# Optimization experiments

Hardware: AMD Instinct MI355X
Metric: run time of the kernel (lower is better)

## Reference

```python
import jax, jax.numpy as jnp
import numpy as np

H = 768
NH = 12
HD = 64
FF = 3072
EPS = 1e-12


def layer_norm(x, g, b):
    mu = jnp.mean(x, axis=-1, keepdims=True)
    var = jnp.mean((x - mu) ** 2, axis=-1, keepdims=True)
    return (x - mu) * jax.lax.rsqrt(var + EPS) * g + b


def setup_inputs() -> dict:
    key = jax.random.key(0)
    ks = jax.random.split(key, 16)
    B, S, L = 16, 512, 50
    s = 0.02
    return {
        "hidden_states": jax.random.normal(ks[0], (B, S, H), jnp.float32),
        "attention_mask": jnp.zeros((B, 1, 1, S), jnp.float32),
        "past_key": jax.random.normal(ks[1], (B, NH, L, HD), jnp.float32),
        "past_value": jax.random.normal(ks[2], (B, NH, L, HD), jnp.float32),
        "Wq": jax.random.normal(ks[3], (H, H), jnp.float32) * s,
        "bq": jnp.zeros((H,), jnp.float32),
        "Wk": jax.random.normal(ks[4], (H, H), jnp.float32) * s,
        "bk": jnp.zeros((H,), jnp.float32),
        "Wv": jax.random.normal(ks[5], (H, H), jnp.float32) * s,
        "bv": jnp.zeros((H,), jnp.float32),
        "Wo": jax.random.normal(ks[6], (H, H), jnp.float32) * s,
        "bo": jnp.zeros((H,), jnp.float32),
        "ln1_g": jnp.ones((H,), jnp.float32),
        "ln1_b": jnp.zeros((H,), jnp.float32),
        "Wi": jax.random.normal(ks[7], (H, FF), jnp.float32) * s,
        "bi": jnp.zeros((FF,), jnp.float32),
        "Wf": jax.random.normal(ks[8], (FF, H), jnp.float32) * s,
        "bf": jnp.zeros((H,), jnp.float32),
        "ln2_g": jnp.ones((H,), jnp.float32),
        "ln2_b": jnp.zeros((H,), jnp.float32),
    }


def reference(hidden_states, attention_mask, past_key, past_value,
              Wq, bq, Wk, bk, Wv, bv, Wo, bo, ln1_g, ln1_b,
              Wi, bi, Wf, bf, ln2_g, ln2_b):
    B, S, _ = hidden_states.shape
    L = past_key.shape[2]

    def heads(x):  # [B,S,H] -> [B,NH,S,HD]
        return x.reshape(B, S, NH, HD).transpose(0, 2, 1, 3)

    q = heads(hidden_states @ Wq + bq)
    k = heads(hidden_states @ Wk + bk)
    v = heads(hidden_states @ Wv + bv)

    # faithful to source bug: past_key_values[0] concatenated into BOTH k and v
    k = jnp.concatenate([past_key, k], axis=2)  # [B,NH,L+S,HD]
    v = jnp.concatenate([past_key, v], axis=2)

    scores = jnp.einsum('bhqd,bhkd->bhqk', q, k) / jnp.sqrt(jnp.float32(HD))
    # visual mask positions get +1.0 (torch.ones), faithful to source
    vis_mask = jnp.ones((B, 1, 1, L), scores.dtype)
    full_mask = jnp.concatenate([vis_mask, attention_mask], axis=-1)
    scores = scores + full_mask

    probs = jax.nn.softmax(scores, axis=-1)
    ctx = jnp.einsum('bhqk,bhkd->bhqd', probs, v)  # [B,NH,S,HD]
    ctx = ctx.transpose(0, 2, 1, 3).reshape(B, S, H)

    attn_out = layer_norm(ctx @ Wo + bo + hidden_states, ln1_g, ln1_b)

    inter = jax.nn.gelu(attn_out @ Wi + bi, approximate=False)
    layer_out = layer_norm(inter @ Wf + bf + attn_out, ln2_g, ln2_b)
    return layer_out
```

## Files before the change

### kernel.cpp

```cpp
#include <hip/hip_runtime.h>
#include <math.h>

#define HDIM 64
#define NHEAD 12
#define HDN 768
#define QKVN 2304
#define FFDIM 3072
#define LPAST 50
#define SEQ 512
#define NBATCH 16
#define TKV (LPAST + SEQ)
#define TKVP 576
#define MTOK (NBATCH * SEQ)
#define NBH (NBATCH * NHEAD)

typedef __attribute__((ext_vector_type(8))) short short8;
typedef __attribute__((ext_vector_type(4))) float f32x4;

__device__ __forceinline__ ushort f2bf(float x) {
    union { float f; unsigned u; } c; c.f = x;
    unsigned r = (c.u + 0x7fffu + ((c.u >> 16) & 1u)) >> 16;
    return (ushort)r;
}
__device__ __forceinline__ float bf2f(ushort u) { return __uint_as_float((unsigned)u << 16); }
__device__ __forceinline__ float geluf(float v) {
    return 0.5f * v * (1.0f + erff(v * 0.70710678118654752f));
}

#define GLOAD_LDS16(gsrc, ldst)                                                    \
    __builtin_amdgcn_global_load_lds(                                              \
        (const __attribute__((address_space(1))) void*)(gsrc),                     \
        (__attribute__((address_space(3))) void*)(ldst), 16, 0, 0)

__global__ __launch_bounds__(256) void cast_bf(const float* __restrict__ x,
                                               ushort* __restrict__ y, int n4) {
    int i = blockIdx.x * 256 + threadIdx.x;
    if (i >= n4) return;
    float4 v = ((const float4*)x)[i];
    ushort4 o; o.x = f2bf(v.x); o.y = f2bf(v.y); o.z = f2bf(v.z); o.w = f2bf(v.w);
    ((ushort4*)y)[i] = o;
}

__global__ __launch_bounds__(256) void pack_bias(const float* __restrict__ bq,
                                                 const float* __restrict__ bk,
                                                 const float* __restrict__ bv,
                                                 float* __restrict__ o) {
    int i = blockIdx.x * 256 + threadIdx.x;
    if (i >= QKVN) return;
    o[i] = i < HDN ? bq[i] : (i < 2 * HDN ? bk[i - HDN] : bv[i - 2 * HDN]);
}

__global__ __launch_bounds__(256) void transpose_cast(const float* __restrict__ W,
                                                      ushort* __restrict__ WT,
                                                      int K, int N) {
    __shared__ float t[32][33];
    const int n0 = blockIdx.x * 32, k0 = blockIdx.y * 32;
    const int tx = threadIdx.x & 31, ty = threadIdx.x >> 5;
    #pragma unroll
    for (int i = 0; i < 4; ++i)
        t[ty + i * 8][tx] = W[(size_t)(k0 + ty + i * 8) * N + n0 + tx];
    __syncthreads();
    #pragma unroll
    for (int i = 0; i < 4; ++i)
        WT[(size_t)(n0 + ty + i * 8) * K + k0 + tx] = f2bf(t[tx][ty + i * 8]);
}

__global__ __launch_bounds__(256) void transpose_cast4(
    const float* __restrict__ W0, const float* __restrict__ W1,
    const float* __restrict__ W2, const float* __restrict__ W3,
    ushort* __restrict__ T0, ushort* __restrict__ T1,
    ushort* __restrict__ T2, ushort* __restrict__ T3) {
    __shared__ float t[32][33];
    const int z = blockIdx.z;
    const float* W = z == 0 ? W0 : z == 1 ? W1 : z == 2 ? W2 : W3;
    ushort* WT = z == 0 ? T0 : z == 1 ? T1 : z == 2 ? T2 : T3;
    const int n0 = blockIdx.x * 32, k0 = blockIdx.y * 32;
    const int tx = threadIdx.x & 31, ty = threadIdx.x >> 5;
    #pragma unroll
    for (int i = 0; i < 4; ++i)
        t[ty + i * 8][tx] = W[(size_t)(k0 + ty + i * 8) * HDN + n0 + tx];
    __syncthreads();
    #pragma unroll
    for (int i = 0; i < 4; ++i)
        WT[(size_t)(n0 + ty + i * 8) * HDN + k0 + tx] = f2bf(t[tx][ty + i * 8]);
}

template<int EPI>
__global__ __launch_bounds__(256) void gemm_mfma3(
    const ushort* __restrict__ A, const ushort* __restrict__ B,
    int lda, int ldb,
    const float* __restrict__ bias, const float* __restrict__ resid,
    const ushort* __restrict__ resid_bf,
    void* __restrict__ Cout, int M, int N, int K)
{
    __shared__ ushort sm[3 * 8192];

    const int tid = threadIdx.x;
    const int lane = tid & 63;
    const int wv = tid >> 6;
    const int wr = wv >> 1, wc = wv & 1;
    const int bm = blockIdx.x * 128, bn = blockIdx.y * 128;
    const int lr = lane & 15, lg = lane >> 4;
    const int swzu = ((lr * 64 + lg * 16) ^ ((lr & 8) << 2)) >> 1;

    int srow[2], skk[2];
    #pragma unroll
    for (int r = 0; r < 2; ++r) {
        int o = (tid + 256 * r) * 16;
        int st = o >> 10;
        int q = o & 1023;
        q ^= ((q >> 9) & 1) << 5;
        srow[r] = st * 16 + (q >> 6);
        skk[r] = (q & 63) >> 1;
    }
    const ushort* Abase = A + (size_t)bm * lda;
    const ushort* Bbase = B + (size_t)bn * ldb;
    const int nt = K >> 5;

    f32x4 acc[4][4] = {};

#define STAGE(T, BUF)                                                            \
    do {                                                                         \
        const int k0_ = (T) << 5;                                                \
        ushort* base_ = sm + (BUF) * 8192;                                       \
        _Pragma("unroll")                                                        \
        for (int r_ = 0; r_ < 2; ++r_) {                                         \
            int sl_ = tid + 256 * r_;                                            \
            GLOAD_LDS16(Abase + (size_t)srow[r_] * lda + k0_ + skk[r_],          \
                        (char*)base_ + sl_ * 16);                                \
        }                                                                        \
        _Pragma("unroll")                                                        \
        for (int r_ = 0; r_ < 2; ++r_) {                                         \
            int sl_ = tid + 256 * r_;                                            \
            GLOAD_LDS16(Bbase + (size_t)srow[r_] * ldb + k0_ + skk[r_],          \
                        (char*)(base_ + 4096) + sl_ * 16);                       \
        }                                                                        \
    } while (0)

    STAGE(0, 0);
    STAGE(1, 1);
    asm volatile("s_waitcnt vmcnt(4)" ::: "memory");
    __builtin_amdgcn_sched_barrier(0);
    __builtin_amdgcn_s_barrier();
    __builtin_amdgcn_sched_barrier(0);

    int buf = 0;
    for (int t = 0; t < nt; ++t) {
        if (t + 2 < nt) {
            int nbuf = buf + 2; if (nbuf >= 3) nbuf -= 3;
            STAGE(t + 2, nbuf);
        }
        const ushort* ab = sm + buf * 8192;
        short8 af[4], bfv[4];
        #pragma unroll
        for (int i = 0; i < 4; ++i) {
            af[i]  = *(const short8*)(ab + (wr * 4 + i) * 512 + swzu);
            bfv[i] = *(const short8*)(ab + 4096 + (wc * 4 + i) * 512 + swzu);
        }
        __builtin_amdgcn_s_setprio(1);
        #pragma unroll
        for (int i = 0; i < 4; ++i)
            #pragma unroll
            for (int j = 0; j < 4; ++j)
                acc[i][j] = __builtin_amdgcn_mfma_f32_16x16x32_bf16(
                    af[i], bfv[j], acc[i][j], 0, 0, 0);
        __builtin_amdgcn_s_setprio(0);
        if (t + 2 < nt)
            asm volatile("s_waitcnt vmcnt(4)" ::: "memory");
        else
            asm volatile("s_waitcnt vmcnt(0)" ::: "memory");
        __builtin_amdgcn_sched_barrier(0);
        __builtin_amdgcn_s_barrier();
        __builtin_amdgcn_sched_barrier(0);
        buf = buf + 1 == 3 ? 0 : buf + 1;
    }
#undef STAGE

    #pragma unroll
    for (int i = 0; i < 4; ++i) {
        #pragma unroll
        for (int j = 0; j < 4; ++j) {
            const int col = bn + wc * 64 + j * 16 + lr;
            const float bv = bias[col];
            #pragma unroll
            for (int rr = 0; rr < 4; ++rr) {
                const int row = bm + wr * 64 + i * 16 + (lane >> 4) * 4 + rr;
                const size_t idx = (size_t)row * N + col;
                float v = acc[i][j][rr] + bv;
                if (EPI == 0) {
                    ((ushort*)Cout)[idx] = f2bf(v);
                } else if (EPI == 1) {
                    ((float*)Cout)[idx] = v + resid[idx];
                } else if (EPI == 2) {
                    ((ushort*)Cout)[idx] = f2bf(geluf(v));
                } else {
                    ((float*)Cout)[idx] = v + bf2f(resid_bf[idx]);
                }
            }
        }
    }
}

__global__ __launch_bounds__(256) void kvK(
    const ushort* __restrict__ qkv, const float* __restrict__ past_key,
    ushort* __restrict__ kf)
{
    const size_t total = (size_t)NBH * TKV * HDIM;
    size_t idx = (size_t)blockIdx.x * 256 + threadIdx.x;
    if (idx >= total) return;
    int d = idx & 63;
    size_t r = idx >> 6;
    int t = (int)(r % TKV);
    int bh = (int)(r / TKV);
    ushort kv_;
    if (t < LPAST) {
        kv_ = f2bf(past_key[((size_t)bh * LPAST + t) * HDIM + d]);
    } else {
        int b = bh / NHEAD, h = bh % NHEAD;
        kv_ = qkv[((size_t)(b * SEQ + (t - LPAST))) * QKVN + HDN + h * HDIM + d];
    }
    kf[idx] = kv_;
}

__global__ __launch_bounds__(256) void kvVT(
    const ushort* __restrict__ qkv, const float* __restrict__ past_key,
    ushort* __restrict__ vt)
{
    __shared__ ushort td[64][72];
    const int bh = blockIdx.x / 9;
    const int t0 = (blockIdx.x % 9) * 64;
    const int b = bh / NHEAD, h = bh % NHEAD;
    const int trow = threadIdx.x >> 2, seg = threadIdx.x & 3;
    const int t = t0 + trow;

    ushort vals[16];
    if (t < LPAST) {
        const float* pk = past_key + ((size_t)bh * LPAST + t) * HDIM + seg * 16;
        #pragma unroll
        for (int i = 0; i < 4; ++i) {
            float4 f = ((const float4*)pk)[i];
            vals[i * 4 + 0] = f2bf(f.x); vals[i * 4 + 1] = f2bf(f.y);
            vals[i * 4 + 2] = f2bf(f.z); vals[i * 4 + 3] = f2bf(f.w);
        }
    } else if (t < TKV) {
        const ushort* vp = qkv + ((size_t)(b * SEQ + (t - LPAST))) * QKVN
                               + 2 * HDN + h * HDIM + seg * 16;
        uint4 u0 = ((const uint4*)vp)[0], u1 = ((const uint4*)vp)[1];
        *(uint4*)&vals[0] = u0; *(uint4*)&vals[8] = u1;
    } else {
        #pragma unroll
        for (int i = 0; i < 16; ++i) vals[i] = 0;
    }
    #pragma unroll
    for (int i = 0; i < 16; ++i) td[trow][seg * 16 + i] = vals[i];
    __syncthreads();

    const int d = threadIdx.x >> 2;
    ushort o[16];
    #pragma unroll
    for (int i = 0; i < 16; ++i) o[i] = td[seg * 16 + i][d];
    ushort* dst = vt + ((size_t)bh * HDIM + d) * TKVP + t0 + seg * 16;
    *(uint4*)dst = *(uint4*)&o[0];
    *(uint4*)(dst + 8) = *(uint4*)&o[8];
}

__global__ __launch_bounds__(256) void attn3(
    const ushort* __restrict__ qkv, const ushort* __restrict__ kf,
    const ushort* __restrict__ vt, const float* __restrict__ mask,
    ushort* __restrict__ ctx)
{
    __shared__ ushort Ks[64 * 64];
    __shared__ ushort Vs[64 * 64];
    __shared__ ushort Ps[4][16 * 64];

    const int wv = threadIdx.x >> 6, lane = threadIdx.x & 63;
    const int lr = lane & 15, lg = lane >> 4;
    const int bid = blockIdx.x;
    const int xcd = bid & 7, gi = bid >> 3;
    const int bh = xcd * (NBH / 8) + (gi >> 3);
    const int s0 = (gi & 7) * 64;
    const int b = bh / NHEAD, h = bh % NHEAD;

    short8 af[2];
    {
        const ushort* qp = qkv + ((size_t)(b * SEQ + s0 + wv * 16 + lr)) * QKVN
                               + h * HDIM + lg * 8;
        af[0] = *(const short8*)qp;
        af[1] = *(const short8*)(qp + 32);
    }

    const ushort* kbase = kf + (size_t)bh * TKV * HDIM;
    const ushort* vbase = vt + (size_t)bh * HDIM * TKVP;

    float m[4] = {-1e30f, -1e30f, -1e30f, -1e30f};
    float l[4] = {};
    f32x4 ctxa[4] = {};

    for (int kt = 0; kt < 9; ++kt) {
        const int t0 = kt * 64;
        #pragma unroll
        for (int r = 0; r < 2; ++r) {
            int sl = (int)threadIdx.x + 256 * r;
            int row = sl >> 3, p = sl & 7;
            int j = p ^ (row & 7);
            int trow = t0 + row; if (trow > TKV - 1) trow = TKV - 1;
            GLOAD_LDS16(kbase + ((size_t)trow << 6) + j * 8, (char*)Ks + sl * 16);
        }
        #pragma unroll
        for (int r = 0; r < 2; ++r) {
            int sl = (int)threadIdx.x + 256 * r;
            int row = sl >> 3, p = sl & 7;
            int j = p ^ (row & 7);
            GLOAD_LDS16(vbase + (size_t)row * TKVP + t0 + j * 8, (char*)Vs + sl * 16);
        }
        __syncthreads();

        f32x4 sa[4] = {};
        #pragma unroll
        for (int kb = 0; kb < 4; ++kb) {
            const int key = kb * 16 + lr;
            #pragma unroll
            for (int c = 0; c < 2; ++c) {
                const int phys = (c * 4 + lg) ^ (key & 7);
                short8 kfrag = *(const short8*)&Ks[key * 64 + phys * 8];
                sa[kb] = __builtin_amdgcn_mfma_f32_16x16x32_bf16(
                    af[c], kfrag, sa[kb], 0, 0, 0);
            }
        }

        float scv[4][4];
        #pragma unroll
        for (int kb = 0; kb < 4; ++kb) {
            const int t = t0 + kb * 16 + lr;
            float add = 0.0f;
            bool dead = (t >= TKV);
            if (!dead) add = (t < LPAST) ? 1.0f : mask[(size_t)b * SEQ + (t - LPAST)];
            #pragma unroll
            for (int r = 0; r < 4; ++r)
                scv[kb][r] = dead ? -1e30f : fmaf(sa[kb][r], 0.125f, add);
        }

        #pragma unroll
        for (int r = 0; r < 4; ++r) {
            float mx = fmaxf(fmaxf(scv[0][r], scv[1][r]), fmaxf(scv[2][r], scv[3][r]));
            mx = fmaxf(mx, __shfl_xor(mx, 1));
            mx = fmaxf(mx, __shfl_xor(mx, 2));
            mx = fmaxf(mx, __shfl_xor(mx, 4));
            mx = fmaxf(mx, __shfl_xor(mx, 8));
            const float mn = fmaxf(m[r], mx);
            const float f = __expf(m[r] - mn);
            m[r] = mn;
            l[r] *= f;
            #pragma unroll
            for (int dg = 0; dg < 4; ++dg) ctxa[dg][r] *= f;
            const int q_ = lg * 4 + r;
            #pragma unroll
            for (int kb = 0; kb < 4; ++kb) {
                float p = __expf(scv[kb][r] - mn);
                l[r] += p;
                const int key = kb * 16 + lr;
                const int phys = (key >> 3) ^ (q_ & 7);
                Ps[wv][q_ * 64 + phys * 8 + (key & 7)] = f2bf(p);
            }
        }

        short8 pa[2];
        #pragma unroll
        for (int c = 0; c < 2; ++c) {
            const int phys = (c * 4 + lg) ^ (lr & 7);
            pa[c] = *(const short8*)&Ps[wv][lr * 64 + phys * 8];
        }
        #pragma unroll
        for (int dg = 0; dg < 4; ++dg) {
            const int d = dg * 16 + lr;
            #pragma unroll
            for (int c = 0; c < 2; ++c) {
                const int phys = (c * 4 + lg) ^ (d & 7);
                short8 vfrag = *(const short8*)&Vs[d * 64 + phys * 8];
                ctxa[dg] = __builtin_amdgcn_mfma_f32_16x16x32_bf16(
                    pa[c], vfrag, ctxa[dg], 0, 0, 0);
            }
        }
        __syncthreads();
    }

    #pragma unroll
    for (int r = 0; r < 4; ++r) {
        float s = l[r];
        s += __shfl_xor(s, 1); s += __shfl_xor(s, 2);
        s += __shfl_xor(s, 4); s += __shfl_xor(s, 8);
        l[r] = 1.0f / s;
    }
    #pragma unroll
    for (int r = 0; r < 4; ++r) {
        const int q_ = s0 + wv * 16 + lg * 4 + r;
        const size_t base = ((size_t)(b * SEQ + q_)) * HDN + h * HDIM;
        #pragma unroll
        for (int dg = 0; dg < 4; ++dg)
            ctx[base + dg * 16 + lr] = f2bf(ctxa[dg][r] * l[r]);
    }
}

__global__ __launch_bounds__(256) void layernorm2(
    const float* __restrict__ x, const float* __restrict__ g,
    const float* __restrict__ b, float* __restrict__ out,
    ushort* __restrict__ out_bf)
{
    const size_t row = blockIdx.x;
    const float* xr = &x[row * HDN];
    const int t = threadIdx.x;

    float v0 = xr[t], v1 = xr[t + 256], v2 = xr[t + 512];

    __shared__ float red[4];
    float s = v0 + v1 + v2;
    #pragma unroll
    for (int off = 32; off > 0; off >>= 1) s += __shfl_xor(s, off);
    if ((t & 63) == 0) red[t >> 6] = s;
    __syncthreads();
    float mean = (red[0] + red[1] + red[2] + red[3]) * (1.0f / 768.0f);

    float d0 = v0 - mean, d1 = v1 - mean, d2 = v2 - mean;
    float vs = d0 * d0 + d1 * d1 + d2 * d2;
    #pragma unroll
    for (int off = 32; off > 0; off >>= 1) vs += __shfl_xor(vs, off);
    __syncthreads();
    if ((t & 63) == 0) red[t >> 6] = vs;
    __syncthreads();
    float var = (red[0] + red[1] + red[2] + red[3]) * (1.0f / 768.0f);
    float rstd = rsqrtf(var + 1e-12f);

    float o0 = d0 * rstd * g[t] + b[t];
    float o1 = d1 * rstd * g[t + 256] + b[t + 256];
    float o2 = d2 * rstd * g[t + 512] + b[t + 512];
    if (out) {
        out[row * HDN + t] = o0;
        out[row * HDN + t + 256] = o1;
        out[row * HDN + t + 512] = o2;
    }
    if (out_bf) {
        out_bf[row * HDN + t] = f2bf(o0);
        out_bf[row * HDN + t + 256] = f2bf(o1);
        out_bf[row * HDN + t + 512] = f2bf(o2);
    }
}

extern "C" void kernel_launch(void* const* d_in, const int* in_sizes, int n_in,
                              void* d_out, int out_size, void* d_ws, size_t ws_size,
                              hipStream_t stream) {
    const float* hs       = (const float*)d_in[0];
    const float* mask     = (const float*)d_in[1];
    const float* past_key = (const float*)d_in[2];
    const float* Wq = (const float*)d_in[4];
    const float* bq = (const float*)d_in[5];
    const float* Wk = (const float*)d_in[6];
    const float* bk = (const float*)d_in[7];
    const float* Wv = (const float*)d_in[8];
    const float* bv = (const float*)d_in[9];
    const float* Wo = (const float*)d_in[10];
    const float* bo = (const float*)d_in[11];
    const float* ln1_g = (const float*)d_in[12];
    const float* ln1_b = (const float*)d_in[13];
    const float* Wi = (const float*)d_in[14];
    const float* bi = (const float*)d_in[15];
    const float* Wf = (const float*)d_in[16];
    const float* bf_ = (const float*)d_in[17];
    const float* ln2_g = (const float*)d_in[18];
    const float* ln2_b = (const float*)d_in[19];
    float* out = (float*)d_out;

    char* w = (char*)d_ws;
    ushort* WqT   = (ushort*)(w + 0);
    ushort* WoT   = (ushort*)(w + 3538944);
    ushort* WiT   = (ushort*)(w + 4718592);
    ushort* WfT   = (ushort*)(w + 9437184);
    float*  bqkv  = (float*)(w + 14155776);
    ushort* hs_bf = (ushort*)(w + 14172160);
    ushort* qkv   = (ushort*)(w + 26755072);
    ushort* kf    = (ushort*)(w + 64503808);
    ushort* vt    = (ushort*)(w + 78315520);
    ushort* ctx_bf = hs_bf;
    float*  tmp   = (float*)(w + 64503808);
    ushort* inter = (ushort*)(w + 14172160);
    ushort* aln_bf = (ushort*)(w + 89669632);
    ushort* WkT = WqT + (size_t)HDN * HDN;
    ushort* WvT = WqT + (size_t)2 * HDN * HDN;

    dim3 b256(256);

    cast_bf<<<dim3((MTOK * HDN / 4 + 255) / 256), b256, 0, stream>>>(hs, hs_bf, MTOK * HDN / 4);
    pack_bias<<<dim3(9), b256, 0, stream>>>(bq, bk, bv, bqkv);
    transpose_cast4<<<dim3(24, 24, 4), b256, 0, stream>>>(Wq, Wk, Wv, Wo, WqT, WkT, WvT, WoT);
    transpose_cast<<<dim3(96, 24), b256, 0, stream>>>(Wi, WiT, HDN, FFDIM);
    transpose_cast<<<dim3(24, 96), b256, 0, stream>>>(Wf, WfT, FFDIM, HDN);

    gemm_mfma3<0><<<dim3(MTOK / 128, QKVN / 128), b256, 0, stream>>>(
        hs_bf, WqT, HDN, HDN, bqkv, nullptr, nullptr, qkv, MTOK, QKVN, HDN);

    {
        size_t ktot = (size_t)NBH * TKV * HDIM;
        kvK<<<dim3((unsigned)((ktot + 255) / 256)), b256, 0, stream>>>(qkv, past_key, kf);
    }
    kvVT<<<dim3(NBH * 9), b256, 0, stream>>>(qkv, past_key, vt);

    attn3<<<dim3(NBH * 8), b256, 0, stream>>>(qkv, kf, vt, mask, ctx_bf);

    gemm_mfma3<1><<<dim3(MTOK / 128, HDN / 128), b256, 0, stream>>>(
        ctx_bf, WoT, HDN, HDN, bo, hs, nullptr, tmp, MTOK, HDN, HDN);
    layernorm2<<<dim3(MTOK), b256, 0, stream>>>(tmp, ln1_g, ln1_b, nullptr, aln_bf);

    gemm_mfma3<2><<<dim3(MTOK / 128, FFDIM / 128), b256, 0, stream>>>(
        aln_bf, WiT, HDN, HDN, bi, nullptr, nullptr, inter, MTOK, FFDIM, HDN);
    gemm_mfma3<4><<<dim3(MTOK / 128, HDN / 128), b256, 0, stream>>>(
        inter, WfT, FFDIM, FFDIM, bf_, nullptr, aln_bf, tmp, MTOK, HDN, FFDIM);

    layernorm2<<<dim3(MTOK), b256, 0, stream>>>(tmp, ln2_g, ln2_b, out, nullptr);
}
```

Measured before the change: 275.1 us.

## Widen GEMM tiles to 128x256, merge prep and KV kernels, bf16 residual temporaries

Five preprocessing launches become one prep kernel, and the K-copy and V-transpose kernels merge into kvAll. The GEMM now uses a 128x256 tile, with each wave covering all 128 rows and 64 columns, held in 72KB of dynamic LDS at two blocks per CU. Residual-sum temporaries for both layernorms move from fp32 to bf16, which halves their memory traffic. The changes aim to cut launch overhead and memory traffic and to raise operand reuse per LDS load, at the cost of more registers, fewer blocks for the N=768 GEMMs, and bf16 rounding before layernorm.

```diff
diff --git a/kernel.cpp b/kernel.cpp
--- a/kernel.cpp
+++ b/kernel.cpp
@@ -32,114 +32,115 @@
         (const __attribute__((address_space(1))) void*)(gsrc),                     \
         (__attribute__((address_space(3))) void*)(ldst), 16, 0, 0)
 
-__global__ __launch_bounds__(256) void cast_bf(const float* __restrict__ x,
-                                               ushort* __restrict__ y, int n4) {
-    int i = blockIdx.x * 256 + threadIdx.x;
-    if (i >= n4) return;
-    float4 v = ((const float4*)x)[i];
-    ushort4 o; o.x = f2bf(v.x); o.y = f2bf(v.y); o.z = f2bf(v.z); o.w = f2bf(v.w);
-    ((ushort4*)y)[i] = o;
-}
-
-__global__ __launch_bounds__(256) void pack_bias(const float* __restrict__ bq,
-                                                 const float* __restrict__ bk,
-                                                 const float* __restrict__ bv,
-                                                 float* __restrict__ o) {
-    int i = blockIdx.x * 256 + threadIdx.x;
-    if (i >= QKVN) return;
-    o[i] = i < HDN ? bq[i] : (i < 2 * HDN ? bk[i - HDN] : bv[i - 2 * HDN]);
-}
-
-__global__ __launch_bounds__(256) void transpose_cast(const float* __restrict__ W,
-                                                      ushort* __restrict__ WT,
-                                                      int K, int N) {
-    __shared__ float t[32][33];
-    const int n0 = blockIdx.x * 32, k0 = blockIdx.y * 32;
-    const int tx = threadIdx.x & 31, ty = threadIdx.x >> 5;
+__global__ __launch_bounds__(256) void prep(
+    const float* __restrict__ hs, ushort* __restrict__ hs_bf,
+    const float* __restrict__ bq, const float* __restrict__ bk,
+    const float* __restrict__ bv, float* __restrict__ bqkv,
+    const float* __restrict__ Wq, const float* __restrict__ Wk,
+    const float* __restrict__ Wv, const float* __restrict__ Wo,
+    ushort* __restrict__ WqT, ushort* __restrict__ WkT,
+    ushort* __restrict__ WvT, ushort* __restrict__ WoT,
+    const float* __restrict__ Wi, ushort* __restrict__ WiT,
+    const float* __restrict__ Wf, ushort* __restrict__ WfT)
+{
+    __shared__ float tls[32][33];
+    int bid = blockIdx.x;
+    const int tid = threadIdx.x;
+
+    if (bid < 6144) {
+        int i = bid * 256 + tid;
+        float4 v = ((const float4*)hs)[i];
+        ushort4 o; o.x = f2bf(v.x); o.y = f2bf(v.y); o.z = f2bf(v.z); o.w = f2bf(v.w);
+        ((ushort4*)hs_bf)[i] = o;
+        return;
+    }
+    bid -= 6144;
+    if (bid < 9) {
+        int i = bid * 256 + tid;
+        bqkv[i] = i < HDN ? bq[i] : (i < 2 * HDN ? bk[i - HDN] : bv[i - 2 * HDN]);
+        return;
+    }
+    bid -= 9;
+
+    const float* W; ushort* WT; int K, N, bx, by;
+    if (bid < 2304) {
+        int z = bid / 576, r = bid % 576;
+        W = z == 0 ? Wq : z == 1 ? Wk : z == 2 ? Wv : Wo;
+        WT = z == 0 ? WqT : z == 1 ? WkT : z == 2 ? WvT : WoT;
+        K = HDN; N = HDN; bx = r % 24; by = r / 24;
+    } else if (bid < 4608) {
+        int r = bid - 2304; W = Wi; WT = WiT; K = HDN; N = FFDIM; bx = r % 96; by = r / 96;
+    } else {
+        int r = bid - 4608; W = Wf; WT = WfT; K = FFDIM; N = HDN; bx = r % 24; by = r / 24;
+    }
+    const int n0 = bx * 32, k0 = by * 32;
+    const int tx = tid & 31, ty = tid >> 5;
     #pragma unroll
     for (int i = 0; i < 4; ++i)
-        t[ty + i * 8][tx] = W[(size_t)(k0 + ty + i * 8) * N + n0 + tx];
+        tls[ty + i * 8][tx] = W[(size_t)(k0 + ty + i * 8) * N + n0 + tx];
     __syncthreads();
     #pragma unroll
     for (int i = 0; i < 4; ++i)
-        WT[(size_t)(n0 + ty + i * 8) * K + k0 + tx] = f2bf(t[tx][ty + i * 8]);
-}
-
-__global__ __launch_bounds__(256) void transpose_cast4(
-    const float* __restrict__ W0, const float* __restrict__ W1,
-    const float* __restrict__ W2, const float* __restrict__ W3,
-    ushort* __restrict__ T0, ushort* __restrict__ T1,
-    ushort* __restrict__ T2, ushort* __restrict__ T3) {
-    __shared__ float t[32][33];
-    const int z = blockIdx.z;
-    const float* W = z == 0 ? W0 : z == 1 ? W1 : z == 2 ? W2 : W3;
-    ushort* WT = z == 0 ? T0 : z == 1 ? T1 : z == 2 ? T2 : T3;
-    const int n0 = blockIdx.x * 32, k0 = blockIdx.y * 32;
-    const int tx = threadIdx.x & 31, ty = threadIdx.x >> 5;
-    #pragma unroll
-    for (int i = 0; i < 4; ++i)
-        t[ty + i * 8][tx] = W[(size_t)(k0 + ty + i * 8) * HDN + n0 + tx];
-    __syncthreads();
-    #pragma unroll
-    for (int i = 0; i < 4; ++i)
-        WT[(size_t)(n0 + ty + i * 8) * HDN + k0 + tx] = f2bf(t[tx][ty + i * 8]);
+        WT[(size_t)(n0 + ty + i * 8) * K + k0 + tx] = f2bf(tls[tx][ty + i * 8]);
 }
 
 template<int EPI>
-__global__ __launch_bounds__(256) void gemm_mfma3(
+__global__ __launch_bounds__(256, 2) void gemm_wide(
     const ushort* __restrict__ A, const ushort* __restrict__ B,
     int lda, int ldb,
     const float* __restrict__ bias, const float* __restrict__ resid,
     const ushort* __restrict__ resid_bf,
-    void* __restrict__ Cout, int M, int N, int K)
+    ushort* __restrict__ Cout, int M, int N, int K)
 {
-    __shared__ ushort sm[3 * 8192];
+    extern __shared__ ushort sm[];
 
     const int tid = threadIdx.x;
     const int lane = tid & 63;
     const int wv = tid >> 6;
-    const int wr = wv >> 1, wc = wv & 1;
-    const int bm = blockIdx.x * 128, bn = blockIdx.y * 128;
+    const int bm = blockIdx.x * 128, bn = blockIdx.y * 256;
     const int lr = lane & 15, lg = lane >> 4;
     const int swzu = ((lr * 64 + lg * 16) ^ ((lr & 8) << 2)) >> 1;
 
-    int srow[2], skk[2];
+    int arow[2], akk[2], brow[4], bkk[4];
     #pragma unroll
     for (int r = 0; r < 2; ++r) {
         int o = (tid + 256 * r) * 16;
-        int st = o >> 10;
-        int q = o & 1023;
+        int st = o >> 10, q = o & 1023;
         q ^= ((q >> 9) & 1) << 5;
-        srow[r] = st * 16 + (q >> 6);
-        skk[r] = (q & 63) >> 1;
+        arow[r] = st * 16 + (q >> 6);
+        akk[r] = (q & 63) >> 1;
+    }
+    #pragma unroll
+    for (int r = 0; r < 4; ++r) {
+        int o = (tid + 256 * r) * 16;
+        int st = o >> 10, q = o & 1023;
+        q ^= ((q >> 9) & 1) << 5;
+        brow[r] = st * 16 + (q >> 6);
+        bkk[r] = (q & 63) >> 1;
     }
     const ushort* Abase = A + (size_t)bm * lda;
     const ushort* Bbase = B + (size_t)bn * ldb;
     const int nt = K >> 5;
 
-    f32x4 acc[4][4] = {};
+    f32x4 acc[8][4] = {};
 
 #define STAGE(T, BUF)                                                            \
     do {                                                                         \
         const int k0_ = (T) << 5;                                                \
-        ushort* base_ = sm + (BUF) * 8192;                                       \
+        char* base_ = (char*)sm + (BUF) * 24576;                                 \
         _Pragma("unroll")                                                        \
-        for (int r_ = 0; r_ < 2; ++r_) {                                         \
-            int sl_ = tid + 256 * r_;                                            \
-            GLOAD_LDS16(Abase + (size_t)srow[r_] * lda + k0_ + skk[r_],          \
-                        (char*)base_ + sl_ * 16);                                \
-        }                                                                        \
+        for (int r_ = 0; r_ < 2; ++r_)                                           \
+            GLOAD_LDS16(Abase + (size_t)arow[r_] * lda + k0_ + akk[r_],          \
+                        base_ + (tid + 256 * r_) * 16);                          \
         _Pragma("unroll")                                                        \
-        for (int r_ = 0; r_ < 2; ++r_) {                                         \
-            int sl_ = tid + 256 * r_;                                            \
-            GLOAD_LDS16(Bbase + (size_t)srow[r_] * ldb + k0_ + skk[r_],          \
-                        (char*)(base_ + 4096) + sl_ * 16);                       \
-        }                                                                        \
+        for (int r_ = 0; r_ < 4; ++r_)                                           \
+            GLOAD_LDS16(Bbase + (size_t)brow[r_] * ldb + k0_ + bkk[r_],          \
+                        base_ + 8192 + (tid + 256 * r_) * 16);                   \
     } while (0)
 
     STAGE(0, 0);
     STAGE(1, 1);
-    asm volatile("s_waitcnt vmcnt(4)" ::: "memory");
+    asm volatile("s_waitcnt vmcnt(6)" ::: "memory");
     __builtin_amdgcn_sched_barrier(0);
     __builtin_amdgcn_s_barrier();
     __builtin_amdgcn_sched_barrier(0);
@@ -150,23 +151,24 @@
             int nbuf = buf + 2; if (nbuf >= 3) nbuf -= 3;
             STAGE(t + 2, nbuf);
         }
-        const ushort* ab = sm + buf * 8192;
-        short8 af[4], bfv[4];
-        #pragma unroll
-        for (int i = 0; i < 4; ++i) {
-            af[i]  = *(const short8*)(ab + (wr * 4 + i) * 512 + swzu);
-            bfv[i] = *(const short8*)(ab + 4096 + (wc * 4 + i) * 512 + swzu);
-        }
+        const ushort* ab = sm + buf * 12288;
+        short8 af[8], bfv[4];
+        #pragma unroll
+        for (int m = 0; m < 8; ++m)
+            af[m] = *(const short8*)(ab + m * 512 + swzu);
+        #pragma unroll
+        for (int n = 0; n < 4; ++n)
+            bfv[n] = *(const short8*)(ab + 4096 + (wv * 4 + n) * 512 + swzu);
         __builtin_amdgcn_s_setprio(1);
         #pragma unroll
-        for (int i = 0; i < 4; ++i)
-            #pragma unroll
-            for (int j = 0; j < 4; ++j)
-                acc[i][j] = __builtin_amdgcn_mfma_f32_16x16x32_bf16(
-                    af[i], bfv[j], acc[i][j], 0, 0, 0);
+        for (int m = 0; m < 8; ++m)
+            #pragma unroll
+            for (int n = 0; n < 4; ++n)
+                acc[m][n] = __builtin_amdgcn_mfma_f32_16x16x32_bf16(
+                    af[m], bfv[n], acc[m][n], 0, 0, 0);
         __builtin_amdgcn_s_setprio(0);
         if (t + 2 < nt)
-            asm volatile("s_waitcnt vmcnt(4)" ::: "memory");
+            asm volatile("s_waitcnt vmcnt(6)" ::: "memory");
         else
             asm volatile("s_waitcnt vmcnt(0)" ::: "memory");
         __builtin_amdgcn_sched_barrier(0);
@@ -177,54 +179,28 @@
 #undef STAGE
 
     #pragma unroll
-    for (int i = 0; i < 4; ++i) {
-        #pragma unroll
-        for (int j = 0; j < 4; ++j) {
-            const int col = bn + wc * 64 + j * 16 + lr;
+    for (int m = 0; m < 8; ++m) {
+        #pragma unroll
+        for (int n = 0; n < 4; ++n) {
+            const int col = bn + wv * 64 + n * 16 + lr;
             const float bv = bias[col];
             #pragma unroll
             for (int rr = 0; rr < 4; ++rr) {
-                const int row = bm + wr * 64 + i * 16 + (lane >> 4) * 4 + rr;
+                const int row = bm + m * 16 + lg * 4 + rr;
                 const size_t idx = (size_t)row * N + col;
-                float v = acc[i][j][rr] + bv;
-                if (EPI == 0) {
-                    ((ushort*)Cout)[idx] = f2bf(v);
-                } else if (EPI == 1) {
-                    ((float*)Cout)[idx] = v + resid[idx];
-                } else if (EPI == 2) {
-                    ((ushort*)Cout)[idx] = f2bf(geluf(v));
-                } else {
-                    ((float*)Cout)[idx] = v + bf2f(resid_bf[idx]);
-                }
+                float v = acc[m][n][rr] + bv;
+                if (EPI == 1) v += resid[idx];
+                if (EPI == 4) v += bf2f(resid_bf[idx]);
+                if (EPI == 2) v = geluf(v);
+                Cout[idx] = f2bf(v);
             }
         }
     }
 }
 
-__global__ __launch_bounds__(256) void kvK(
+__global__ __launch_bounds__(256) void kvAll(
     const ushort* __restrict__ qkv, const float* __restrict__ past_key,
-    ushort* __restrict__ kf)
-{
-    const size_t total = (size_t)NBH * TKV * HDIM;
-    size_t idx = (size_t)blockIdx.x * 256 + threadIdx.x;
-    if (idx >= total) return;
-    int d = idx & 63;
-    size_t r = idx >> 6;
-    int t = (int)(r % TKV);
-    int bh = (int)(r / TKV);
-    ushort kv_;
-    if (t < LPAST) {
-        kv_ = f2bf(past_key[((size_t)bh * LPAST + t) * HDIM + d]);
-    } else {
-        int b = bh / NHEAD, h = bh % NHEAD;
-        kv_ = qkv[((size_t)(b * SEQ + (t - LPAST))) * QKVN + HDN + h * HDIM + d];
-    }
-    kf[idx] = kv_;
-}
-
-__global__ __launch_bounds__(256) void kvVT(
-    const ushort* __restrict__ qkv, const float* __restrict__ past_key,
-    ushort* __restrict__ vt)
+    ushort* __restrict__ kf, ushort* __restrict__ vt)
 {
     __shared__ ushort td[64][72];
     const int bh = blockIdx.x / 9;
@@ -233,26 +209,38 @@
     const int trow = threadIdx.x >> 2, seg = threadIdx.x & 3;
     const int t = t0 + trow;
 
-    ushort vals[16];
+    ushort kv16[16], vv16[16];
     if (t < LPAST) {
         const float* pk = past_key + ((size_t)bh * LPAST + t) * HDIM + seg * 16;
         #pragma unroll
         for (int i = 0; i < 4; ++i) {
             float4 f = ((const float4*)pk)[i];
-            vals[i * 4 + 0] = f2bf(f.x); vals[i * 4 + 1] = f2bf(f.y);
-            vals[i * 4 + 2] = f2bf(f.z); vals[i * 4 + 3] = f2bf(f.w);
-        }
+            kv16[i * 4 + 0] = f2bf(f.x); kv16[i * 4 + 1] = f2bf(f.y);
+            kv16[i * 4 + 2] = f2bf(f.z); kv16[i * 4 + 3] = f2bf(f.w);
+        }
+        #pragma unroll
+        for (int i = 0; i < 16; ++i) vv16[i] = kv16[i];
     } else if (t < TKV) {
-        const ushort* vp = qkv + ((size_t)(b * SEQ + (t - LPAST))) * QKVN
-                               + 2 * HDN + h * HDIM + seg * 16;
-        uint4 u0 = ((const uint4*)vp)[0], u1 = ((const uint4*)vp)[1];
-        *(uint4*)&vals[0] = u0; *(uint4*)&vals[8] = u1;
+        const ushort* kp = qkv + ((size_t)(b * SEQ + (t - LPAST))) * QKVN
+                               + HDN + h * HDIM + seg * 16;
+        *(uint4*)&kv16[0] = ((const uint4*)kp)[0];
+        *(uint4*)&kv16[8] = ((const uint4*)kp)[1];
+        const ushort* vp = kp + HDN;
+        *(uint4*)&vv16[0] = ((const uint4*)vp)[0];
+        *(uint4*)&vv16[8] = ((const uint4*)vp)[1];
     } else {
         #pragma unroll
-        for (int i = 0; i < 16; ++i) vals[i] = 0;
-    }
-    #pragma unroll
-    for (int i = 0; i < 16; ++i) td[trow][seg * 16 + i] = vals[i];
+        for (int i = 0; i < 16; ++i) { kv16[i] = 0; vv16[i] = 0; }
+    }
+
+    if (t < TKV) {
+        ushort* kd = kf + (((size_t)bh * TKV + t) << 6) + seg * 16;
+        *(uint4*)kd = *(uint4*)&kv16[0];
+        *(uint4*)(kd + 8) = *(uint4*)&kv16[8];
+    }
+
+    #pragma unroll
+    for (int i = 0; i < 16; ++i) td[trow][seg * 16 + i] = vv16[i];
     __syncthreads();
 
     const int d = threadIdx.x >> 2;
@@ -401,16 +389,16 @@
     }
 }
 
-__global__ __launch_bounds__(256) void layernorm2(
-    const float* __restrict__ x, const float* __restrict__ g,
+__global__ __launch_bounds__(256) void layernorm3(
+    const ushort* __restrict__ x, const float* __restrict__ g,
     const float* __restrict__ b, float* __restrict__ out,
     ushort* __restrict__ out_bf)
 {
     const size_t row = blockIdx.x;
-    const float* xr = &x[row * HDN];
+    const ushort* xr = &x[row * HDN];
     const int t = threadIdx.x;
 
-    float v0 = xr[t], v1 = xr[t + 256], v2 = xr[t + 512];
+    float v0 = bf2f(xr[t]), v1 = bf2f(xr[t + 256]), v2 = bf2f(xr[t + 512]);
 
     __shared__ float red[4];
     float s = v0 + v1 + v2;
@@ -480,39 +468,42 @@
     ushort* kf    = (ushort*)(w + 64503808);
     ushort* vt    = (ushort*)(w + 78315520);
     ushort* ctx_bf = hs_bf;
-    float*  tmp   = (float*)(w + 64503808);
-    ushort* inter = (ushort*)(w + 14172160);
+    ushort* tmp_bf = (ushort*)(w + 64503808);
+    ushort* inter  = (ushort*)(w + 14172160);
     ushort* aln_bf = (ushort*)(w + 89669632);
     ushort* WkT = WqT + (size_t)HDN * HDN;
     ushort* WvT = WqT + (size_t)2 * HDN * HDN;
 
     dim3 b256(256);
 
-    cast_bf<<<dim3((MTOK * HDN / 4 + 255) / 256), b256, 0, stream>>>(hs, hs_bf, MTOK * HDN / 4);
-    pack_bias<<<dim3(9), b256, 0, stream>>>(bq, bk, bv, bqkv);
-    transpose_cast4<<<dim3(24, 24, 4), b256, 0, stream>>>(Wq, Wk, Wv, Wo, WqT, WkT, WvT, WoT);
-    transpose_cast<<<dim3(96, 24), b256, 0, stream>>>(Wi, WiT, HDN, FFDIM);
-    transpose_cast<<<dim3(24, 96), b256, 0, stream>>>(Wf, WfT, FFDIM, HDN);
-
-    gemm_mfma3<0><<<dim3(MTOK / 128, QKVN / 128), b256, 0, stream>>>(
+    hipFuncSetAttribute((const void*)&gemm_wide<0>,
+                        hipFuncAttributeMaxDynamicSharedMemorySize, 73728);
+    hipFuncSetAttribute((const void*)&gemm_wide<1>,
+                        hipFuncAttributeMaxDynamicSharedMemorySize, 73728);
+    hipFuncSetAttribute((const void*)&gemm_wide<2>,
+                        hipFuncAttributeMaxDynamicSharedMemorySize, 73728);
+    hipFuncSetAttribute((const void*)&gemm_wide<4>,
+                        hipFuncAttributeMaxDynamicSharedMemorySize, 73728);
+
+    prep<<<dim3(13065), b256, 0, stream>>>(
+        hs, hs_bf, bq, bk, bv, bqkv,
+        Wq, Wk, Wv, Wo, WqT, WkT, WvT, WoT, Wi, WiT, Wf, WfT);
+
+    gemm_wide<0><<<dim3(MTOK / 128, QKVN / 256), b256, 73728, stream>>>(
         hs_bf, WqT, HDN, HDN, bqkv, nullptr, nullptr, qkv, MTOK, QKVN, HDN);
 
-    {
-        size_t ktot = (size_t)NBH * TKV * HDIM;
-        kvK<<<dim3((unsigned)((ktot + 255) / 256)), b256, 0, stream>>>(qkv, past_key, kf);
-    }
-    kvVT<<<dim3(NBH * 9), b256, 0, stream>>>(qkv, past_key, vt);
+    kvAll<<<dim3(NBH * 9), b256, 0, stream>>>(qkv, past_key, kf, vt);
 
     attn3<<<dim3(NBH * 8), b256, 0, stream>>>(qkv, kf, vt, mask, ctx_bf);
 
-    gemm_mfma3<1><<<dim3(MTOK / 128, HDN / 128), b256, 0, stream>>>(
-        ctx_bf, WoT, HDN, HDN, bo, hs, nullptr, tmp, MTOK, HDN, HDN);
-    layernorm2<<<dim3(MTOK), b256, 0, stream>>>(tmp, ln1_g, ln1_b, nullptr, aln_bf);
-
-    gemm_mfma3<2><<<dim3(MTOK / 128, FFDIM / 128), b256, 0, stream>>>(
+    gemm_wide<1><<<dim3(MTOK / 128, HDN / 256), b256, 73728, stream>>>(
+        ctx_bf, WoT, HDN, HDN, bo, hs, nullptr, tmp_bf, MTOK, HDN, HDN);
+    layernorm3<<<dim3(MTOK), b256, 0, stream>>>(tmp_bf, ln1_g, ln1_b, nullptr, aln_bf);
+
+    gemm_wide<2><<<dim3(MTOK / 128, FFDIM / 256), b256, 73728, stream>>>(
         aln_bf, WiT, HDN, HDN, bi, nullptr, nullptr, inter, MTOK, FFDIM, HDN);
-    gemm_mfma3<4><<<dim3(MTOK / 128, HDN / 128), b256, 0, stream>>>(
-        inter, WfT, FFDIM, FFDIM, bf_, nullptr, aln_bf, tmp, MTOK, HDN, FFDIM);
-
-    layernorm2<<<dim3(MTOK), b256, 0, stream>>>(tmp, ln2_g, ln2_b, out, nullptr);
-}
+    gemm_wide<4><<<dim3(MTOK / 128, HDN / 256), b256, 73728, stream>>>(
+        inter, WfT, FFDIM, FFDIM, bf_, nullptr, aln_bf, tmp_bf, MTOK, HDN, FFDIM);
+
+    layernorm3<<<dim3(MTOK), b256, 0, stream>>>(tmp_bf, ln2_g, ln2_b, out, nullptr);
+}
```

Measured after the change: 278.6 us. About the same (+1.3%).
